# Kernel tuning notes

Measured on AMD Instinct MI355X. Metric: run time of the kernel, lower is better.

The kernel has to match this reference:

```python
import jax, jax.numpy as jnp
import numpy as np
from math import ceil

N, C_IN, HV, WV = 4, 3, 256, 256
C, K, NUM_LAYERS = 16, 3, 10
HK, WK = 45, 45
PROX_SCALE, KSCALE, KBSCALE, EPS = 10.0, 100.0, 0.01, 1e-8


def conv2_same(x, w):
    # torch F.conv2d (cross-correlation) with 'same' padding
    return jax.lax.conv_general_dilated(x, w, (1, 1), 'SAME',
                                        dimension_numbers=('NCHW', 'OIHW', 'NCHW'))


def pad_to(x, size):
    h, w = x.shape[-2], x.shape[-1]
    pads = [(0, 0)] * (x.ndim - 2) + [(0, size[0] - h), (0, size[1] - w)]
    return jnp.pad(x, pads)


def soft_threshold(x, b):
    return jnp.sign(x) * jax.nn.relu(jnp.abs(x) - b)


def circ_shift(x, s):
    return jnp.roll(x, (-s[0], -s[1]), axis=(-2, -1))


def csq(c):
    return (c * jnp.conj(c)).real


def forward(blurred_image, w0, ws, biases, kernel_biases, kernel_proxes, zetas, eta):
    Nb, C_in, Hv, Wv = blurred_image.shape
    Hs, Ws = Hv + HK - 1, Wv + WK - 1
    Hb, Wb = Hs + HK - 1, Ws + WK - 1
    fft_size = (int(ceil(Hb / 64.0) * 64), int(ceil(Wb / 64.0) * 64))
    rfft = lambda x: jnp.fft.rfft2(x, s=fft_size, axes=(-2, -1))
    irfft = lambda X: jnp.fft.irfft2(X, s=fft_size, axes=(-2, -1))

    # first-layer filter: zero-mean per (out,in) filter, then spatial reflect
    w_mean = w0.reshape(C, C_in, -1).mean(axis=-1)
    w0c = w0 - w_mean[:, :, None, None]
    w0_unreflected = jnp.transpose(w0c, (1, 0, 2, 3))   # (C_in, C, K, K)
    w0r = w0c[:, :, ::-1, ::-1]

    # analysis: cascade of convs, each feature stack padded to fft_size
    wy_list = []
    fy = blurred_image
    for layer in range(NUM_LAYERS):
        w = w0r if layer == 0 else ws[layer - 1]
        fy = conv2_same(fy, w)
        fy_p = pad_to(jnp.pad(fy, ((0, 0), (0, 0), (HK - 1, HK - 1), (WK - 1, WK - 1))), fft_size)
        wy_list.append(fy_p)

    delta = jnp.zeros((Nb, HK, WK), dtype=blurred_image.dtype).at[:, HK // 2, WK // 2].set(1.0)
    b0 = biases[0][None, :, None, None]
    z = soft_threshold(circ_shift(wy_list[-1], (HK // 2, WK // 2)), b0)
    Fz = rfft(z)
    k = delta
    Fg = None
    for layer in range(NUM_LAYERS):
        fy_p = wy_list.pop()
        Ffy = rfft(fy_p)                       # (N, C, H, Wf) complex
        Fk = rfft(k)[:, None]                  # (N, 1, H, Wf)
        zeta = PROX_SCALE * zetas[layer][None, :, None, None]
        num = zeta * (jnp.conj(Fk) * Ffy) + Fz
        den = zeta * csq(Fk) + 1.0
        Fg = num / (den + EPS)
        b = biases[layer + 1][None, :, None, None]
        z = soft_threshold(irfft(Fg), b)
        Fz = rfft(z)
        zk = kernel_proxes[layer]
        num_k = zk * jnp.sum(jnp.conj(Fz) * Ffy, axis=1) + Fk[:, 0]
        den_k = zk * jnp.sum(csq(Fz), axis=1) + 1.0
        k = irfft(num_k / (den_k + EPS))
        k_flat = k.reshape(Nb, -1)
        k_max = jax.scipy.special.logsumexp(k_flat * KSCALE, axis=-1) / KSCALE
        bk = KBSCALE * kernel_biases[layer]
        k = jax.nn.relu(k[:, :HK, :WK] - bk * k_max[:, None, None])
        k_sum = jnp.sum(k, axis=(1, 2), keepdims=True)
        k = (k + EPS * delta) / (k_sum + EPS)

    # final closed-form image solve in frequency domain (3-channel Cramer's rule)
    Fy = rfft(jnp.pad(blurred_image, ((0, 0), (0, 0), (HK - 1, HK - 1), (WK - 1, WK - 1))))
    Fk = rfft(k)                                # (N, H, Wf)
    Fw0 = rfft(circ_shift(pad_to(w0_unreflected, fft_size), (K // 2, K // 2)))  # (C_in, C, H, Wf)
    b_final = biases[NUM_LAYERS + 1][None, :, None, None]
    Fg = rfft(soft_threshold(irfft(Fg), b_final))

    eta_s = PROX_SCALE * eta[None, :, None, None]      # (1, C, 1, 1)
    Fwr, Fwg, Fwb = Fw0[0:1], Fw0[1:2], Fw0[2:3]       # (1, C, H, Wf)
    Fyr, Fyg, Fyb = Fy[:, 0], Fy[:, 1], Fy[:, 2]
    Fk_sq = csq(Fk)
    Crr = Fk_sq + jnp.sum(eta_s * csq(Fwr), axis=1)
    Cgg = Fk_sq + jnp.sum(eta_s * csq(Fwg), axis=1)
    Cbb = Fk_sq + jnp.sum(eta_s * csq(Fwb), axis=1)
    Crg = jnp.sum(eta_s * jnp.conj(Fwr) * Fwg, axis=1)
    Crb = jnp.sum(eta_s * jnp.conj(Fwr) * Fwb, axis=1)
    Cgb = jnp.sum(eta_s * jnp.conj(Fwg) * Fwb, axis=1)
    Fk_conj = jnp.conj(Fk)
    Br = Fk_conj * Fyr + jnp.sum(eta_s * jnp.conj(Fwr) * Fg, axis=1)
    Bg = Fk_conj * Fyg + jnp.sum(eta_s * jnp.conj(Fwg) * Fg, axis=1)
    Bb = Fk_conj * Fyb + jnp.sum(eta_s * jnp.conj(Fwb) * Fg, axis=1)
    Crg_sq, Crb_sq, Cgb_sq = csq(Crg), csq(Crb), csq(Cgb)
    Irr = Cgg * Cbb - Cgb_sq
    Igg = Crr * Cbb - Crb_sq
    Ibb = Crr * Cgg - Crg_sq
    Irg = jnp.conj(Cgb) * Crb - Cbb * Crg
    Irb = Crg * Cgb - Cgg * Crb
    Igb = jnp.conj(Crg) * Crb - Crr * Cgb
    den = (Crr * (Cgg * Cbb - Cgb_sq) - Cgg * Crb_sq - Cbb * Crg_sq
           + 2 * (Crg * Cgb * jnp.conj(Crb)).real) + EPS
    Fxr = Irr * Br + Irg * Bg + Irb * Bb
    Fxg = jnp.conj(Irg) * Br + Igg * Bg + Igb * Bb
    Fxb = jnp.conj(Irb) * Br + jnp.conj(Igb) * Bg + Ibb * Bb
    Fx = jnp.stack([Fxr, Fxg, Fxb], axis=1) / den[:, None]

    image = irfft(Fx)[:, :, HK // 2:HK // 2 + Hv, WK // 2:WK // 2 + Wv]
    return image, k


def setup_inputs() -> dict:
    key = jax.random.key(0)
    ks = jax.random.split(key, 4)

    def xavier(k, shape, fan_in, fan_out):
        std = (2.0 / (fan_in + fan_out)) ** 0.5
        return std * jax.random.normal(k, shape, dtype=jnp.float32)

    return {
        'blurred_image': jax.random.normal(ks[0], (N, C_IN, HV, WV), dtype=jnp.float32),
        'w0': xavier(ks[1], (C, C_IN, K, K), C_IN * K * K, C * K * K),
        'ws': xavier(ks[2], (NUM_LAYERS - 1, C, C, 3, 3), C * 9, C * 9),
        'biases': jnp.full((NUM_LAYERS + 2, C), 0.02, dtype=jnp.float32),
        'kernel_biases': jnp.zeros((NUM_LAYERS,), dtype=jnp.float32),
        'kernel_proxes': jnp.ones((NUM_LAYERS,), dtype=jnp.float32),
        'zetas': jnp.ones((NUM_LAYERS, C), dtype=jnp.float32),
        'eta': jnp.ones((C,), dtype=jnp.float32),
    }


def reference(blurred_image, w0, ws, biases, kernel_biases, kernel_proxes, zetas, eta):
    return forward(blurred_image, w0, ws, biases, kernel_biases, kernel_proxes, zetas, eta)
```

## Files before the change

kernel.cpp:

```cpp
#include <hip/hip_runtime.h>
#include <math.h>

#define FH 384
#define KF 193
#define KS 384
#define SPW 147456

typedef __attribute__((ext_vector_type(8))) short short8;
typedef __attribute__((ext_vector_type(4))) float f32x4;
typedef unsigned int u32;
typedef unsigned short u16;

static __device__ __forceinline__ float softt(float v, float b) {
    return copysignf(fmaxf(fabsf(v) - b, 0.f), v);
}
static __device__ __forceinline__ u16 bf16_rn(float v) {
    u32 u = __float_as_uint(v);
    u32 r = (u + 0x7FFFu + ((u >> 16) & 1u)) >> 16;
    return (u16)r;
}
static __device__ __forceinline__ float bf16_to_f(u16 h) {
    return __uint_as_float(((u32)h) << 16);
}
static __device__ __forceinline__ float2 ldc(const uint2* __restrict__ S, size_t i) {
    uint2 u = S[i];
    float2 r;
    r.x = __uint_as_float((u.x & 0xffffu) << 16) + __uint_as_float((u.y & 0xffffu) << 16);
    r.y = __uint_as_float(u.x & 0xffff0000u) + __uint_as_float(u.y & 0xffff0000u);
    return r;
}
static __device__ __forceinline__ uint2 packc(float re, float im) {
    u16 hr = bf16_rn(re), hi = bf16_rn(im);
    u16 lr = bf16_rn(re - bf16_to_f(hr)), li = bf16_rn(im - bf16_to_f(hi));
    uint2 o; o.x = (u32)hr | ((u32)hi << 16); o.y = (u32)lr | ((u32)li << 16);
    return o;
}

__global__ void init_ef_k(float2* Ef) {
    int idx = blockIdx.x * 256 + threadIdx.x;
    if (idx >= FH * FH) return;
    int h = idx / FH, j = idx % FH;
    int m = (h * j) % FH;
    float th = (float)(6.283185307179586 / FH) * (float)m;
    float2 v; v.x = cosf(th); v.y = -sinf(th);
    Ef[idx] = v;
}

__global__ void init_tw(float2* twT) {
    int i = blockIdx.x * 256 + threadIdx.x;
    if (i < 193) {
        float th = (float)(6.283185307179586 / 384.0) * (float)i;
        float2 v; v.x = cosf(th); v.y = sinf(th);
        twT[i] = v;
    }
}

__global__ void init_estack192(u16* __restrict__ H, u16* __restrict__ L, int inv)
{
    int idx = blockIdx.x * 256 + threadIdx.x;
    if (idx >= KS * KS) return;
    int gm = idx / KS, kp = idx % KS;
    int m = gm >> 1, comp = gm & 1;
    int t = kp >> 1, ri = kp & 1;
    int mm = (m * t) % 192;
    float th = (float)(6.283185307179586 / 192.0) * (float)mm;
    float c = cosf(th), s = sinf(th);
    float er, ei;
    if (inv) { er = c * (1.f/384.f); ei = s * (1.f/384.f); }
    else     { er = c;               ei = -s; }
    float v;
    if (comp == 0) v = (ri == 0) ? er : -ei;
    else           v = (ri == 0) ? ei :  er;
    u16 h = bf16_rn(v);
    H[idx] = h;
    L[idx] = bf16_rn(v - bf16_to_f(h));
}

__global__ void init_t192(u16* __restrict__ H, u16* __restrict__ L)
{
    int idx = blockIdx.x * 256 + threadIdx.x;
    if (idx >= 208 * 192) return;
    int n = idx / 192, m = idx % 192;
    float v = 0.f;
    if (n < 194) {
        int j = n >> 1, ri = n & 1;
        int mm = (j * m) % 192;
        float th = (float)(6.283185307179586 / 192.0) * (float)mm;
        v = ri ? -sinf(th) : cosf(th);
    }
    u16 h = bf16_rn(v);
    H[idx] = h;
    L[idx] = bf16_rn(v - bf16_to_f(h));
}

__global__ void init_u192(u16* __restrict__ H, u16* __restrict__ L)
{
    int idx = blockIdx.x * 256 + threadIdx.x;
    if (idx >= 192 * 224) return;
    int m = idx / 224, kk = idx % 224;
    float v = 0.f;
    if (kk < 194) {
        int j = kk >> 1, ri = kk & 1;
        float cj = (j == 0 || j == 96) ? (1.f/384.f) : (2.f/384.f);
        int mm = (j * m) % 192;
        float th = (float)(6.283185307179586 / 192.0) * (float)mm;
        v = ri ? -cj*sinf(th) : cj*cosf(th);
    }
    u16 h = bf16_rn(v);
// ... 249 lines not shown
#pragma unroll
    for (int mi = 0; mi < 2; ++mi)
#pragma unroll
        for (int nj = 0; nj < 4; ++nj) {
            accA[mi][nj] = (f32x4){0.f,0.f,0.f,0.f};
            accB[mi][nj] = (f32x4){0.f,0.f,0.f,0.f};
        }
    const u16* hP = Hs + (size_t)plane*inH*inW;
    const u16* lP = Ls + (size_t)plane*inH*inW;
    int W2  = inW >> 1;
    int ox2 = offX >> 1;
    bool al16 = ((ox2 & 7) == 0);
    int mhi = (offX + inW) >> 1;
    for (int kt = 0; kt < mhi; kt += 32) {
#pragma unroll
        for (int s = 0; s < 4; ++s) {
            int slot = tid + s*256;
            int p    = slot >> 9;
            int inr  = slot & 511;
            int r = inr >> 2, kq2 = inr & 3;
            int yy = y0 + r - offY;
            int m0 = kt + kq2*8;
            int pos = m0 - ox2;
            uint4 hq = {0u,0u,0u,0u}, lq4 = {0u,0u,0u,0u};
            if (yy >= 0 && yy < inH) {
                const u16* hr = hP + (size_t)yy*inW + (size_t)p*W2;
                const u16* lr = lP + (size_t)yy*inW + (size_t)p*W2;
                if (pos >= 0 && pos + 8 <= W2) {
                    if (al16) {
                        hq  = *(const uint4*)(hr + pos);
                        lq4 = *(const uint4*)(lr + pos);
                    } else {
                        hq.x = *(const u32*)(hr+pos);   hq.y = *(const u32*)(hr+pos+2);
                        hq.z = *(const u32*)(hr+pos+4); hq.w = *(const u32*)(hr+pos+6);
                        lq4.x = *(const u32*)(lr+pos);   lq4.y = *(const u32*)(lr+pos+2);
                        lq4.z = *(const u32*)(lr+pos+4); lq4.w = *(const u32*)(lr+pos+6);
                    }
                } else if (pos + 8 > 0 && pos < W2) {
#pragma unroll
                    for (int q = 0; q < 4; ++q) {
                        int pp = pos + 2*q;
                        if (pp >= 0 && pp + 2 <= W2) {
                            ((u32*)&hq)[q]  = *(const u32*)(hr+pp);
                            ((u32*)&lq4)[q] = *(const u32*)(lr+pp);
                        }
                    }
                }
            }
            int base = ((r >> 4)*64 + (r & 15) + 16*kq2)*8;
            *(uint4*)&AhS[p][base] = hq;
            *(uint4*)&AlS[p][base] = lq4;
        }
        __syncthreads();
        short8 A0h[2], A0l[2], A1h[2], A1l[2];
#pragma unroll
        for (int mi = 0; mi < 2; ++mi) {
            int fo = ((wave*2 + mi)*64 + lane)*8;
            A0h[mi] = *(const short8*)&AhS[0][fo];
            A0l[mi] = *(const short8*)&AlS[0][fo];
            A1h[mi] = *(const short8*)&AhS[1][fo];
            A1l[mi] = *(const short8*)&AlS[1][fo];
        }
#pragma unroll
        for (int nj = 0; nj < 4; ++nj) {
            if (nj >= njN) continue;
            size_t toff = (size_t)(col0 + nj*16 + lm)*192 + kt + lq*8;
            short8 Bh = *(const short8*)(TH + toff);
            short8 Bl = *(const short8*)(TL + toff);
#pragma unroll
            for (int mi = 0; mi < 2; ++mi) {
                accA[mi][nj] = __builtin_amdgcn_mfma_f32_16x16x32_bf16(A0h[mi], Bh, accA[mi][nj], 0, 0, 0);
                accA[mi][nj] = __builtin_amdgcn_mfma_f32_16x16x32_bf16(A0h[mi], Bl, accA[mi][nj], 0, 0, 0);
                accA[mi][nj] = __builtin_amdgcn_mfma_f32_16x16x32_bf16(A0l[mi], Bh, accA[mi][nj], 0, 0, 0);
                accB[mi][nj] = __builtin_amdgcn_mfma_f32_16x16x32_bf16(A1h[mi], Bh, accB[mi][nj], 0, 0, 0);
                accB[mi][nj] = __builtin_amdgcn_mfma_f32_16x16x32_bf16(A1h[mi], Bl, accB[mi][nj], 0, 0, 0);
                accB[mi][nj] = __builtin_amdgcn_mfma_f32_16x16x32_bf16(A1l[mi], Bh, accB[mi][nj], 0, 0, 0);
            }
        }
        __syncthreads();
    }
    r2c192_epilogue(accA, accB, col0, njN, y0, wave, lm, lq, twT, outp, B, plane);
}

__global__ void gpm_kernel(uint2* __restrict__ S, const float2* __restrict__ twT, int rows)
{
    int idx = blockIdx.x*256 + threadIdx.x;
    if (idx >= rows * 97) return;
    int j = idx % 97;
    size_t b = (size_t)(idx / 97) * KF;
    if (j == 96) {
        float2 f = ldc(S, b + 96);
        S[b + 96] = packc(2.f*f.x, -2.f*f.y);
    } else {
        float2 f1 = ldc(S, b + j);
        float2 f2 = ldc(S, b + 192 - j);
        float gpx = f1.x + f2.x, gpy = f1.y - f2.y;
        float hx  = f1.x - f2.x, hy  = f1.y + f2.y;
        float2 tw = twT[j];
        float gmx = tw.x*hx - tw.y*hy;
        float gmy = tw.x*hy + tw.y*hx;
        S[b + j]       = packc(gpx, gpy);
        S[b + 192 - j] = packc(gmx, gmy);
    }
}

__global__ __launch_bounds__(256) void c2r192(
    const uint2* __restrict__ Ain,
    const u16* __restrict__ UH, const u16* __restrict__ UL,
    float* __restrict__ outp, const float* __restrict__ thr,
    u16* __restrict__ spH, u16* __restrict__ spL, int B)
{
    __shared__ u16 AhS[2][8*64*8];
    __shared__ u16 AlS[2][8*64*8];
    int col0 = blockIdx.x * 64;
    int y0   = blockIdx.y * 128;
    int plane = blockIdx.z;
    int tid = threadIdx.x;
    int wave = tid >> 6, lane = tid & 63;
    int lm = lane & 15, lq = lane >> 4;
    f32x4 accP[2][4], accQ[2][4];
#pragma unroll
    for (int mi = 0; mi < 2; ++mi)
#pragma unroll
        for (int nj = 0; nj < 4; ++nj) {
            accP[mi][nj] = (f32x4){0.f,0.f,0.f,0.f};
            accQ[mi][nj] = (f32x4){0.f,0.f,0.f,0.f};
        }
    for (int kt = 0; kt < 194; kt += 32) {
#pragma unroll
        for (int s = 0; s < 8; ++s) {
            int slot = tid + s*256;
            int p   = slot >> 10;
            int inr = slot & 1023;
            int r = inr >> 3, kq = inr & 7;
            size_t rowb = ((size_t)(y0 + r)*B + plane)*KF;
            int j0 = (kt + kq*4) >> 1;
            uint2 u0, u1;
            u0.x = u0.y = u1.x = u1.y = 0u;
            if (p == 0) {
                if (j0 < 96) u0 = Ain[rowb + j0];
                else if (j0 == 96) {
                    uint2 t = Ain[rowb + 96];
                    u0.x = t.x & 0xffffu; u0.y = t.y & 0xffffu;
                }
                if (j0 + 1 < 96) u1 = Ain[rowb + j0 + 1];
            } else {
                if (j0 < 96) u0 = Ain[rowb + 192 - j0];
                else if (j0 == 96) {
                    uint2 t = Ain[rowb + 96];
                    u0.x = t.x >> 16; u0.y = t.y >> 16;
                }
                if (j0 + 1 < 96) u1 = Ain[rowb + 191 - j0];
            }
            int base = ((r >> 4)*64 + (r & 15) + 16*(kq >> 1))*8 + (kq & 1)*4;
            uint2 hp, lp;
            hp.x = u0.x; hp.y = u1.x;
            lp.x = u0.y; lp.y = u1.y;
            *(uint2*)&AhS[p][base] = hp;
            *(uint2*)&AlS[p][base] = lp;
        }
        __syncthreads();
        short8 A0h[2], A0l[2], A1h[2], A1l[2];
#pragma unroll
        for (int mi = 0; mi < 2; ++mi) {
            int fo = ((wave*2 + mi)*64 + lane)*8;
            A0h[mi] = *(const short8*)&AhS[0][fo];
            A0l[mi] = *(const short8*)&AlS[0][fo];
            A1h[mi] = *(const short8*)&AhS[1][fo];
            A1l[mi] = *(const short8*)&AlS[1][fo];
        }
#pragma unroll
        for (int nj = 0; nj < 4; ++nj) {
            size_t toff = (size_t)(col0 + nj*16 + lm)*224 + kt + lq*8;
            short8 Bh = *(const short8*)(UH + toff);
            short8 Bl = *(const short8*)(UL + toff);
#pragma unroll
            for (int mi = 0; mi < 2; ++mi) {
                accP[mi][nj] = __builtin_amdgcn_mfma_f32_16x16x32_bf16(A0h[mi], Bh, accP[mi][nj], 0, 0, 0);
                accP[mi][nj] = __builtin_amdgcn_mfma_f32_16x16x32_bf16(A0h[mi], Bl, accP[mi][nj], 0, 0, 0);
                accP[mi][nj] = __builtin_amdgcn_mfma_f32_16x16x32_bf16(A0l[mi], Bh, accP[mi][nj], 0, 0, 0);
                accQ[mi][nj] = __builtin_amdgcn_mfma_f32_16x16x32_bf16(A1h[mi], Bh, accQ[mi][nj], 0, 0, 0);
                accQ[mi][nj] = __builtin_amdgcn_mfma_f32_16x16x32_bf16(A1h[mi], Bl, accQ[mi][nj], 0, 0, 0);
                accQ[mi][nj] = __builtin_amdgcn_mfma_f32_16x16x32_bf16(A1l[mi], Bh, accQ[mi][nj], 0, 0, 0);
            }
        }
        __syncthreads();
    }
    float bthr = thr ? thr[plane & 15] : 0.f;
#pragma unroll
    for (int mi = 0; mi < 2; ++mi) {
#pragma unroll
        for (int nj = 0; nj < 4; ++nj) {
            int m = col0 + nj*16 + lm;
#pragma unroll
            for (int rr = 0; rr < 4; ++rr) {
                int y = y0 + wave*32 + mi*16 + lq*4 + rr;
                float xe = accP[mi][nj][rr];
                float xo = accQ[mi][nj][rr];
                float2 o2; o2.x = xe; o2.y = xo;
                *(float2*)&outp[((size_t)plane*FH + y)*FH + 2*m] = o2;
                if (spH) {
                    float s0 = softt(xe, bthr), s1 = softt(xo, bthr);
                    u16 h0 = bf16_rn(s0), h1 = bf16_rn(s1);
                    u16 l0 = bf16_rn(s0 - bf16_to_f(h0)), l1 = bf16_rn(s1 - bf16_to_f(h1));
                    size_t d = (size_t)plane*SPW + (size_t)y*FH + m;
                    spH[d]       = h0; spL[d]       = l0;
                    spH[d + 192] = h1; spL[d + 192] = l1;
                }
            }
        }
    }
}

__global__ __launch_bounds__(256) void zgemm_col_mfma2(
    const u16* __restrict__ EH, const u16* __restrict__ EL,
    const uint2* __restrict__ Bm, uint2* __restrict__ Cm, int N, float sgn,
    int ktHi, const float2* __restrict__ twT)
{
    __shared__ u16 BhS[2][4*64*8];
    __shared__ u16 BlS[2][4*64*8];
    int col0 = blockIdx.x * 64;
    int row0 = blockIdx.y * 128;
    int tid = threadIdx.x;
    int wave = tid >> 6, lane = tid & 63;
    int lm = lane & 15, lq = lane >> 4;
    f32x4 accE[2][4], accO[2][4];
#pragma unroll
    for (int mi = 0; mi < 2; ++mi)
#pragma unroll
        for (int nj = 0; nj < 4; ++nj) {
            accE[mi][nj] = (f32x4){0.f,0.f,0.f,0.f};
            accO[mi][nj] = (f32x4){0.f,0.f,0.f,0.f};
        }
    int arow0 = row0 + wave*32 + lm;
    for (int kt = 0; kt < ktHi; kt += 32) {
        int tbase = kt >> 1;
#pragma unroll
        for (int s = 0; s < 4; ++s) {
            int slot = tid + s*256;
            int p    = slot >> 9;
            int inr  = slot & 511;
            int pair = inr >> 6;
            int n    = inr & 63;
            int gn   = col0 + n;
            int t0   = tbase + pair*2;
            uint2 u0, u1;
            u0.x = u0.y = u1.x = u1.y = 0u;
            if (gn < N) {
                u0 = Bm[(size_t)(2*t0 + p)*N + gn];
                u1 = Bm[(size_t)(2*t0 + 2 + p)*N + gn];
            }
            int ntile = n >> 4, n0 = n & 15;
            int lrow  = (pair >> 1)*16 + n0;
            int base  = (ntile*64 + lrow)*8 + (pair & 1)*4;
            uint2 hp, lp;
            hp.x = u0.x; hp.y = u1.x;
            lp.x = u0.y; lp.y = u1.y;
            *(uint2*)&BhS[p][base] = hp;
            *(uint2*)&BlS[p][base] = lp;
        }
        __syncthreads();
        short8 Ah[2], Al[2];
#pragma unroll
        for (int mi = 0; mi < 2; ++mi) {
            size_t aoff = (size_t)(arow0 + mi*16)*KS + kt + lq*8;
            Ah[mi] = *(const short8*)(EH + aoff);
            Al[mi] = *(const short8*)(EL + aoff);
        }
#pragma unroll
        for (int nj = 0; nj < 4; ++nj) {
            short8 Bh0 = *(const short8*)&BhS[0][(nj*64 + lane)*8];
            short8 Bl0 = *(const short8*)&BlS[0][(nj*64 + lane)*8];
            short8 Bh1 = *(const short8*)&BhS[1][(nj*64 + lane)*8];
            short8 Bl1 = *(const short8*)&BlS[1][(nj*64 + lane)*8];
#pragma unroll
            for (int mi = 0; mi < 2; ++mi) {
                accE[mi][nj] = __builtin_amdgcn_mfma_f32_16x16x32_bf16(Ah[mi], Bh0, accE[mi][nj], 0, 0, 0);
                accE[mi][nj] = __builtin_amdgcn_mfma_f32_16x16x32_bf16(Ah[mi], Bl0, accE[mi][nj], 0, 0, 0);
                accE[mi][nj] = __builtin_amdgcn_mfma_f32_16x16x32_bf16(Al[mi], Bh0, accE[mi][nj], 0, 0, 0);
                accO[mi][nj] = __builtin_amdgcn_mfma_f32_16x16x32_bf16(Ah[mi], Bh1, accO[mi][nj], 0, 0, 0);
                accO[mi][nj] = __builtin_amdgcn_mfma_f32_16x16x32_bf16(Ah[mi], Bl1, accO[mi][nj], 0, 0, 0);
                accO[mi][nj] = __builtin_amdgcn_mfma_f32_16x16x32_bf16(Al[mi], Bh1, accO[mi][nj], 0, 0, 0);
            }
        }
        __syncthreads();
    }
#pragma unroll
    for (int mi = 0; mi < 2; ++mi) {
#pragma unroll
        for (int nj = 0; nj < 4; ++nj) {
            int coln = col0 + nj*16 + lm;
            if (coln < N) {
                int r0 = row0 + wave*32 + mi*16 + lq*4;
                int h  = r0 >> 1;
#pragma unroll
                for (int pp = 0; pp < 2; ++pp) {
                    float e_re = accE[mi][nj][2*pp],   e_im = accE[mi][nj][2*pp+1];
                    float o_re = accO[mi][nj][2*pp],   o_im = accO[mi][nj][2*pp+1];
                    int hh = h + pp;
                    float2 tw = twT[hh];
                    float twr = tw.x, twi = sgn * tw.y;
                    float tr = twr*o_re - twi*o_im;
                    float ti = twr*o_im + twi*o_re;
                    Cm[(size_t)hh*N + coln]         = packc(e_re + tr, e_im + ti);
                    Cm[(size_t)(hh + 192)*N + coln] = packc(e_re - tr, e_im - ti);
                }
            }
        }
    }
}

__global__ void fg_kernel(const uint2* __restrict__ Ffy, uint2* __restrict__ Fz,
                          const uint2* __restrict__ Fk, const float* __restrict__ zetas,
                          int L, int total)
{
    int idx = blockIdx.x*256 + threadIdx.x;
    if (idx >= total) return;
    int k = idx % KF; int r = idx / KF;
    int c = r & 15; int hi = r >> 4;
    float zeta = 10.f * zetas[L*16 + c];
    float2 fk = ldc(Fk, (size_t)hi*KF + k);
    float2 fy = ldc(Ffy, idx);
    float2 fz = ldc(Fz, idx);
    float nx = zeta*(fk.x*fy.x + fk.y*fy.y) + fz.x;
    float ny = zeta*(fk.x*fy.y - fk.y*fy.x) + fz.y;
    float den = zeta*(fk.x*fk.x + fk.y*fk.y) + 1.f + 1e-8f;
    float inv = 1.f/den;
    Fz[idx] = packc(nx*inv, ny*inv);
}

__global__ void knum_kernel(const uint2* __restrict__ Fz, const uint2* __restrict__ Ffy,
                            const uint2* __restrict__ Fk, const float* __restrict__ kprox,
                            int L, int total, uint2* __restrict__ outk)
{
    int idx = blockIdx.x*256 + threadIdx.x;
    if (idx >= total) return;
    int k = idx % KF; int r = idx / KF;
    float zk = kprox[L];
    float s1x = 0.f, s1y = 0.f, s2 = 0.f;
    for (int c = 0; c < 16; ++c) {
        size_t bi = ((size_t)r*16 + c)*KF + k;
        float2 fz = ldc(Fz, bi), fy = ldc(Ffy, bi);
        s1x += fz.x*fy.x + fz.y*fy.y;
        s1y += fz.x*fy.y - fz.y*fy.x;
        s2  += fz.x*fz.x + fz.y*fz.y;
    }
    float2 fk = ldc(Fk, idx);
    float nx = zk*s1x + fk.x, ny = zk*s1y + fk.y;
    float den = zk*s2 + 1.f + 1e-8f;
    float inv = 1.f/den;
    outk[idx] = packc(nx*inv, ny*inv);
}

__device__ __forceinline__ void lse_comb(float& m, float& s, float m2, float s2)
{
    if (m2 > m) { s = s * expf(m - m2) + s2; m = m2; }
    else        { s = s + s2 * expf(m2 - m); }
}

__global__ __launch_bounds__(256) void lse_part_kernel(const float* __restrict__ kraw0,
                                                       float2* __restrict__ parts)
{
    int img = blockIdx.y;
    const float* kraw = kraw0 + (size_t)img*FH*FH;
    int b = blockIdx.x, t = threadIdx.x;
    float m = -1e30f, s = 0.f;
    for (int i = b*256 + t; i < FH*FH; i += 64*256) {
        float v = 100.f * kraw[i];
        lse_comb(m, s, v, 1.f);
    }
    __shared__ float sm[256], ss[256];
    sm[t] = m; ss[t] = s;
    __syncthreads();
    for (int st = 128; st > 0; st >>= 1) {
        if (t < st) {
            float mm = sm[t], sc = ss[t];
            lse_comb(mm, sc, sm[t+st], ss[t+st]);
            sm[t] = mm; ss[t] = sc;
        }
        __syncthreads();
    }
    if (t == 0) { float2 o; o.x = sm[0]; o.y = ss[0]; parts[img*64 + b] = o; }
}

__global__ void zero_kernel(float* __restrict__ p, int n)
{
    int i = blockIdx.x*256 + threadIdx.x;
    if (i < n) p[i] = 0.f;
}

__global__ void kdelta_kernel(float* __restrict__ kful, int G)
{
    int t = threadIdx.x;
    if (t < G) kful[(size_t)t*FH*FH + 22*FH + 22] = 1.f;
}

__global__ __launch_bounds__(256) void knew_kernel(const float2* __restrict__ parts,
    const float* __restrict__ kraw0, const float* __restrict__ kb, int L,
    float* __restrict__ kful0)
{
    int img = blockIdx.x;
    const float* kraw = kraw0 + (size_t)img*FH*FH;
    float*       kful = kful0 + (size_t)img*FH*FH;
    int t = threadIdx.x;
    __shared__ float sm[64], ss[64];
    if (t < 64) { float2 p = parts[img*64 + t]; sm[t] = p.x; ss[t] = p.y; }
    __syncthreads();
    for (int st = 32; st > 0; st >>= 1) {
        if (t < st) {
            float mm = sm[t], sc = ss[t];
            lse_comb(mm, sc, sm[t+st], ss[t+st]);
            sm[t] = mm; ss[t] = sc;
        }
        __syncthreads();
    }
    float kmax = (sm[0] + logf(ss[0])) * 0.01f;
    float thr = 0.01f * kb[L] * kmax;
    float vs[8]; float loc = 0.f;
#pragma unroll
    for (int ii = 0; ii < 8; ++ii) {
        int i = t + ii*256;
        float v = 0.f;
        if (i < 45*45) {
            int y = i/45, x = i - y*45;
            v = fmaxf(kraw[y*FH + x] - thr, 0.f);
        }
        vs[ii] = v; loc += v;
    }
    __shared__ float sr[256];
    sr[t] = loc; __syncthreads();
    for (int st = 128; st > 0; st >>= 1) { if (t < st) sr[t] += sr[t+st]; __syncthreads(); }
    float den = sr[0] + 1e-8f;
#pragma unroll
    for (int ii = 0; ii < 8; ++ii) {
        int i = t + ii*256;
        if (i < 45*45) {
            int y = i/45, x = i - y*45;
            float v = vs[ii] + ((y == 22 && x == 22) ? 1e-8f : 0.f);
            kful[y*FH + x] = v / den;
        }
    }
}

__global__ void fw0_kernel(const float* __restrict__ w0c, const float2* __restrict__ Ef,
                           float2* __restrict__ Fw0)
{
    int idx = blockIdx.x*256 + threadIdx.x;
    if (idx >= 48*FH*KF) return;
    int k = idx % KF; int r = idx / KF;
    int c = r & 15; int r2 = r >> 4;
    int ci = r2 % 3; int h = r2 / 3;
    float accx = 0.f, accy = 0.f;
#pragma unroll
    for (int ky = 0; ky < 3; ++ky) {
        int a1 = ky - 1; if (a1 < 0) a1 += FH;
        float2 e1 = Ef[h*FH + a1];
#pragma unroll
        for (int kx = 0; kx < 3; ++kx) {
            int a2 = kx - 1; if (a2 < 0) a2 += FH;
            float2 e2 = Ef[k*FH + a2];
            float wv = w0c[((c*3 + ci)*3 + ky)*3 + kx];
            float tr = e1.x*e2.x - e1.y*e2.y;
            float ti = e1.x*e2.y + e1.y*e2.x;
            accx += wv*tr; accy += wv*ti;
        }
    }
    float2 o; o.x = accx; o.y = accy;
    Fw0[idx] = o;
}

__global__ void wiener_kernel(const uint2* __restrict__ Fk, const uint2* __restrict__ Fy,
    const float2* __restrict__ Fw0, const uint2* __restrict__ Fg2,
    const float* __restrict__ eta, int G, int total, uint2* __restrict__ Fx)
{
    int idx = blockIdx.x*256 + threadIdx.x;
    if (idx >= total) return;
    int k = idx % KF; int r = idx / KF;
    int h = r / G;
    float2 fk = ldc(Fk, idx);
    float fksq = fk.x*fk.x + fk.y*fk.y;
    float2 fyr = ldc(Fy, ((size_t)3*r + 0)*KF + k);
    float2 fyg = ldc(Fy, ((size_t)3*r + 1)*KF + k);
    float2 fyb = ldc(Fy, ((size_t)3*r + 2)*KF + k);
    float Crr = fksq, Cgg = fksq, Cbb = fksq;
    float2 Crg, Crb, Cgb;
    Crg.x = Crg.y = Crb.x = Crb.y = Cgb.x = Cgb.y = 0.f;
    float2 Br, Bg, Bb;
    Br.x = fk.x*fyr.x + fk.y*fyr.y; Br.y = fk.x*fyr.y - fk.y*fyr.x;
    Bg.x = fk.x*fyg.x + fk.y*fyg.y; Bg.y = fk.x*fyg.y - fk.y*fyg.x;
    Bb.x = fk.x*fyb.x + fk.y*fyb.y; Bb.y = fk.x*fyb.y - fk.y*fyb.x;
    for (int c = 0; c < 16; ++c) {
// ... 6 lines not shown
        Cgg += es*(wg.x*wg.x + wg.y*wg.y);
        Cbb += es*(wb.x*wb.x + wb.y*wb.y);
        Crg.x += es*(wr.x*wg.x + wr.y*wg.y); Crg.y += es*(wr.x*wg.y - wr.y*wg.x);
        Crb.x += es*(wr.x*wb.x + wr.y*wb.y); Crb.y += es*(wr.x*wb.y - wr.y*wb.x);
        Cgb.x += es*(wg.x*wb.x + wg.y*wb.y); Cgb.y += es*(wg.x*wb.y - wg.y*wb.x);
        Br.x += es*(wr.x*g.x + wr.y*g.y); Br.y += es*(wr.x*g.y - wr.y*g.x);
        Bg.x += es*(wg.x*g.x + wg.y*g.y); Bg.y += es*(wg.x*g.y - wg.y*g.x);
        Bb.x += es*(wb.x*g.x + wb.y*g.y); Bb.y += es*(wb.x*g.y - wb.y*g.x);
    }
    float Crg_sq = Crg.x*Crg.x + Crg.y*Crg.y;
    float Crb_sq = Crb.x*Crb.x + Crb.y*Crb.y;
    float Cgb_sq = Cgb.x*Cgb.x + Cgb.y*Cgb.y;
    float Irr = Cgg*Cbb - Cgb_sq;
    float Igg = Crr*Cbb - Crb_sq;
    float Ibb = Crr*Cgg - Crg_sq;
    float2 Irg, Irb, Igb;
    Irg.x = (Cgb.x*Crb.x + Cgb.y*Crb.y) - Cbb*Crg.x;
    Irg.y = (Cgb.x*Crb.y - Cgb.y*Crb.x) - Cbb*Crg.y;
    Irb.x = (Crg.x*Cgb.x - Crg.y*Cgb.y) - Cgg*Crb.x;
    Irb.y = (Crg.x*Cgb.y + Crg.y*Cgb.x) - Cgg*Crb.y;
    Igb.x = (Crg.x*Crb.x + Crg.y*Crb.y) - Crr*Cgb.x;
    Igb.y = (Crg.x*Crb.y - Crg.y*Crb.x) - Crr*Cgb.y;
    float tx_ = Crg.x*Cgb.x - Crg.y*Cgb.y;
    float ty_ = Crg.x*Cgb.y + Crg.y*Cgb.x;
    float den = Crr*Irr - Cgg*Crb_sq - Cbb*Crg_sq + 2.f*(tx_*Crb.x + ty_*Crb.y) + 1e-8f;
    float inv = 1.f/den;
    float ox, oy;
    ox = (Irr*Br.x + (Irg.x*Bg.x - Irg.y*Bg.y) + (Irb.x*Bb.x - Irb.y*Bb.y))*inv;
    oy = (Irr*Br.y + (Irg.x*Bg.y + Irg.y*Bg.x) + (Irb.x*Bb.y + Irb.y*Bb.x))*inv;
    Fx[((size_t)3*r + 0)*KF + k] = packc(ox, oy);
    ox = ((Irg.x*Br.x + Irg.y*Br.y) + Igg*Bg.x + (Igb.x*Bb.x - Igb.y*Bb.y))*inv;
    oy = ((Irg.x*Br.y - Irg.y*Br.x) + Igg*Bg.y + (Igb.x*Bb.y + Igb.y*Bb.x))*inv;
    Fx[((size_t)3*r + 1)*KF + k] = packc(ox, oy);
    ox = ((Irb.x*Br.x + Irb.y*Br.y) + (Igb.x*Bg.x + Igb.y*Bg.y) + Ibb*Bb.x)*inv;
    oy = ((Irb.x*Br.y - Irb.y*Br.x) + (Igb.x*Bg.y - Igb.y*Bg.x) + Ibb*Bb.y)*inv;
    Fx[((size_t)3*r + 2)*KF + k] = packc(ox, oy);
}

__global__ void crop_kernel(const float* __restrict__ sp, float* __restrict__ outp, int total)
{
    int idx = blockIdx.x*256 + threadIdx.x;
    if (idx >= total) return;
    int x = idx & 255; int r = idx >> 8; int y = r & 255; int plane = r >> 8;
    outp[idx] = sp[((size_t)plane*FH + (y+22))*FH + (x+22)];
}

__global__ void kcopy_kernel(const float* __restrict__ kful, float* __restrict__ outp, int total)
{
    int idx = blockIdx.x*256 + threadIdx.x;
    if (idx >= total) return;
    int rem = idx % 2025; int img = idx / 2025;
    int x = rem % 45; int y = rem / 45;
    outp[idx] = kful[(size_t)img*FH*FH + y*FH + x];
}

extern "C" void kernel_launch(void* const* d_in, const int* in_sizes, int n_in,
                              void* d_out, int out_size, void* d_ws, size_t ws_size,
                              hipStream_t stream)
{
    (void)in_sizes; (void)n_in; (void)out_size;
    const float* blurred = (const float*)d_in[0];
    const float* w0      = (const float*)d_in[1];
    const float* wsw     = (const float*)d_in[2];
    const float* biases  = (const float*)d_in[3];
    const float* kbias   = (const float*)d_in[4];
    const float* kprox   = (const float*)d_in[5];
    const float* zetas   = (const float*)d_in[6];
    const float* eta     = (const float*)d_in[7];
    float* outp = (float*)d_out;

    auto al = [](size_t b) { return (b + 255) & ~(size_t)255; };
    auto need = [&](int G) -> size_t {
        size_t s = 0;
        s += al((size_t)FH*FH*8);
        s += al(193*8);
        s += 4*al((size_t)KS*KS*2);
        s += 2*al((size_t)208*192*2);
        s += 2*al((size_t)192*224*2);
        s += al(432*4);
        s += 2*al((size_t)10*G*16*65536*2);
        s += al((size_t)G*16*FH*FH*4);
        s += 2*al((size_t)G*16*SPW*2);
        s += 3*al((size_t)G*16*FH*KF*8);
        s += 3*al((size_t)G*FH*KF*8);
        s += 2*al((size_t)G*FH*FH*4);
        s += 2*al((size_t)G*3*FH*KF*8);
        s += al((size_t)G*64*8);
        return s;
    };
    int G = 4;
    while (G > 1 && need(G) > ws_size) G >>= 1;

    char* base = (char*)d_ws;
    size_t off = 0;
    auto alloc = [&](size_t bytes) -> void* {
        void* p = (void*)(base + off);
        off += (bytes + 255) & ~(size_t)255;
        return p;
    };
    float2* Ef   = (float2*)alloc((size_t)FH*FH*8);
    float2* twT  = (float2*)alloc(193*8);
    u16* EfH = (u16*)alloc((size_t)KS*KS*2);
    u16* EfL = (u16*)alloc((size_t)KS*KS*2);
    u16* EiH = (u16*)alloc((size_t)KS*KS*2);
    u16* EiL = (u16*)alloc((size_t)KS*KS*2);
    u16* T1H = (u16*)alloc((size_t)208*192*2);
    u16* T1L = (u16*)alloc((size_t)208*192*2);
    u16* U1H = (u16*)alloc((size_t)192*224*2);
    u16* U1L = (u16*)alloc((size_t)192*224*2);
    float*  w0cB = (float*)alloc(432*4);
    u16*    fyH  = (u16*)alloc((size_t)10*G*16*65536*2);
    u16*    fyL  = (u16*)alloc((size_t)10*G*16*65536*2);
    float*  zsp  = (float*)alloc((size_t)G*16*FH*FH*4);
    u16*    zspSH= (u16*)alloc((size_t)G*16*SPW*2);
    u16*    zspSL= (u16*)alloc((size_t)G*16*SPW*2);
    uint2*  mid  = (uint2*)alloc((size_t)G*16*FH*KF*8);
    uint2*  FzFg = (uint2*)alloc((size_t)G*16*FH*KF*8);
    uint2*  Ffy  = (uint2*)alloc((size_t)G*16*FH*KF*8);
    uint2*  Fk   = (uint2*)alloc((size_t)G*FH*KF*8);
    uint2*  kfA  = (uint2*)alloc((size_t)G*FH*KF*8);
    uint2*  kfB  = (uint2*)alloc((size_t)G*FH*KF*8);
    float*  kraw = (float*)alloc((size_t)G*FH*FH*4);
    float*  kful = (float*)alloc((size_t)G*FH*FH*4);
    uint2*  FyB  = (uint2*)alloc((size_t)G*3*FH*KF*8);
    uint2*  FxB  = (uint2*)alloc((size_t)G*3*FH*KF*8);
    float2* lseP = (float2*)alloc((size_t)G*64*8);
    float2* Fw0B = (float2*)fyH;

    init_ef_k<<<(FH*FH+255)/256, 256, 0, stream>>>(Ef);
    init_tw<<<1, 256, 0, stream>>>(twT);
    init_estack192<<<(KS*KS+255)/256, 256, 0, stream>>>(EfH, EfL, 0);
    init_estack192<<<(KS*KS+255)/256, 256, 0, stream>>>(EiH, EiL, 1);
    init_t192<<<(208*192+255)/256, 256, 0, stream>>>(T1H, T1L);
    init_u192<<<(192*224+255)/256, 256, 0, stream>>>(U1H, U1L);
    w0c_kernel<<<1, 64, 0, stream>>>(w0, w0cB);

    auto zgf = [&](const uint2* Bm, uint2* Cm, int Ncols) {
        zgemm_col_mfma2<<<dim3((Ncols+63)/64, 3), 256, 0, stream>>>(
            EfH, EfL, Bm, Cm, Ncols, -1.f, KS, twT);
    };
    auto zgi = [&](const uint2* Bm, uint2* Cm, int Ncols) {
        zgemm_col_mfma2<<<dim3((Ncols+63)/64, 3), 256, 0, stream>>>(
            EiH, EiL, Bm, Cm, Ncols, 1.f, KS, twT);
    };
    auto r2c = [&](const float* inp, int inH, int inW, int oY, int oX,
                   const float* thr, uint2* o, int B) {
        r2c192_f<<<dim3(4, 3, B), 256, 0, stream>>>(
            inp, inH, inW, inW, (size_t)inH*inW, oY, oX, thr, T1H, T1L, twT, o, B);
    };
    auto r2cs = [&](const u16* Hs, const u16* Ls, int inH, int inW, int oY, int oX,
                    uint2* o, int B) {
        r2c192_s<<<dim3(4, 3, B), 256, 0, stream>>>(
            Hs, Ls, inH, inW, oY, oX, T1H, T1L, twT, o, B);
    };
    auto c2r = [&](uint2* Ain, float* o, int B,
                   const float* thr, u16* sH, u16* sL) {
        int rows = FH * B;
        gpm_kernel<<<(rows*97 + 255)/256, 256, 0, stream>>>(Ain, twT, rows);
        c2r192<<<dim3(3, 3, B), 256, 0, stream>>>(
            Ain, U1H, U1L, o, thr, sH, sL, B);
    };
    auto r2ck = [&]() {
        r2c192_f<<<dim3(4, 1, G), 256, 0, stream>>>(
            kful, 45, 45, FH, (size_t)FH*FH, 0, 0, nullptr, T1H, T1L, twT, mid, G);
        zgemm_col_mfma2<<<dim3((G*KF+63)/64, 3), 256, 0, stream>>>(
            EfH, EfL, mid, Fk, G*KF, -1.f, 64, twT);
    };

    const size_t CKL = (size_t)G*16*65536;

    for (int g0 = 0; g0 < 4; g0 += G) {
        const float* img = blurred + (size_t)g0*3*65536;

        conv3x3_kernel<<<dim3(16,16,G), 256, 0, stream>>>(
            img, nullptr, nullptr, w0cB, fyH, fyL, 3, 1, (size_t)3*65536);
        for (int l = 1; l < 10; ++l)
            conv3x3_kernel<<<dim3(16,16,G), 256, 0, stream>>>(
                nullptr, fyH + (size_t)(l-1)*CKL, fyL + (size_t)(l-1)*CKL,
                wsw + (size_t)(l-1)*2304,
                fyH + (size_t)l*CKL, fyL + (size_t)l*CKL, 16, 0, (size_t)16*65536);

        int totZ = G*16*FH*FH;
        zinit_kernel<<<(totZ+255)/256, 256, 0, stream>>>(
            fyH + 9*CKL, fyL + 9*CKL, biases, zspSH, zspSL, totZ);
        r2cs(zspSH, zspSL, FH, FH, 0, 0, mid, G*16);
        zgf(mid, FzFg, G*16*KF);

        zero_kernel<<<(G*FH*FH+255)/256, 256, 0, stream>>>(kful, G*FH*FH);
        kdelta_kernel<<<1, 64, 0, stream>>>(kful, G);

        int totS = G*16*FH*KF;
        int totK = G*FH*KF;
        for (int it = 0; it < 10; ++it) {
            int Lfy = 9 - it;
            r2cs(fyH + (size_t)Lfy*CKL, fyL + (size_t)Lfy*CKL, 256, 256, 44, 44, mid, G*16);
            zgf(mid, Ffy, G*16*KF);
            r2ck();
            fg_kernel<<<(totS+255)/256, 256, 0, stream>>>(Ffy, FzFg, Fk, zetas, it, totS);
            zgi(FzFg, mid, G*16*KF);
            c2r(mid, zsp, G*16, biases + (it+1)*16, zspSH, zspSL);
            r2cs(zspSH, zspSL, FH, FH, 0, 0, mid, G*16);
            zgf(mid, FzFg, G*16*KF);
            knum_kernel<<<(totK+255)/256, 256, 0, stream>>>(FzFg, Ffy, Fk, kprox, it, totK, kfA);
            zgi(kfA, kfB, G*KF);
            c2r(kfB, kraw, G, nullptr, nullptr, nullptr);
            lse_part_kernel<<<dim3(64,G), 256, 0, stream>>>(kraw, lseP);
            knew_kernel<<<G, 256, 0, stream>>>(lseP, kraw, kbias, it, kful);
        }

        r2c(img, 256, 256, 44, 44, nullptr, mid, 3*G);
        zgf(mid, FyB, 3*G*KF);
        r2ck();
        r2c(zsp, FH, FH, 0, 0, biases + 11*16, mid, G*16);
        zgf(mid, FzFg, G*16*KF);
        fw0_kernel<<<(48*FH*KF+255)/256, 256, 0, stream>>>(w0cB, Ef, Fw0B);
        wiener_kernel<<<(totK+255)/256, 256, 0, stream>>>(Fk, FyB, Fw0B, FzFg, eta, G, totK, FxB);
        zgi(FxB, mid, 3*G*KF);
        c2r(mid, zsp, 3*G, nullptr, nullptr, nullptr);
        int totC = G*3*65536;
        crop_kernel<<<(totC+255)/256, 256, 0, stream>>>(zsp, outp + (size_t)g0*3*65536, totC);
        int totKC = G*2025;
        kcopy_kernel<<<(totKC+255)/256, 256, 0, stream>>>(kful, outp + 786432 + g0*2025, totKC);
    }
}
```

Measured before the change: 8.726 ms.

## Fuse fg update into column FFT epilogue and LSE partials into c2r

Folds the per-element Fz/Fg Wiener-style update into the epilogue of the forward column FFT GEMM for Ffy, which removes the separate fg_kernel launch and its reread of Ffy. Folds the log-sum-exp partial reduction into the c2r192 epilogue and drops lse_part_kernel, so knew combines 9 partials per image instead of 64. Moves the kernel-FFT r2ck ahead and gives it its own scratch buffer (kmid) so it no longer overwrites mid. It also precomputes the per-slot load indices outside the k loop. The cost is extra registers and global loads in the GEMM epilogue, plus a shared-memory reduction at the end of c2r.

```diff
diff --git a/kernel.cpp b/kernel.cpp
--- a/kernel.cpp
+++ b/kernel.cpp
@@ -24,6 +24,12 @@
 }
 static __device__ __forceinline__ float2 ldc(const uint2* __restrict__ S, size_t i) {
     uint2 u = S[i];
+    float2 r;
+    r.x = __uint_as_float((u.x & 0xffffu) << 16) + __uint_as_float((u.y & 0xffffu) << 16);
+    r.y = __uint_as_float(u.x & 0xffff0000u) + __uint_as_float(u.y & 0xffff0000u);
+    return r;
+}
+static __device__ __forceinline__ float2 ldcu(uint2 u) {
     float2 r;
     r.x = __uint_as_float((u.x & 0xffffu) << 16) + __uint_as_float((u.y & 0xffffu) << 16);
     r.y = __uint_as_float(u.x & 0xffff0000u) + __uint_as_float(u.y & 0xffff0000u);
@@ -439,6 +445,12 @@
     r2c192_epilogue(accA, accB, col0, njN, y0, wave, lm, lq, twT, outp, B, plane);
 }
 
+__device__ __forceinline__ void lse_comb(float& m, float& s, float m2, float s2)
+{
+    if (m2 > m) { s = s * expf(m - m2) + s2; m = m2; }
+    else        { s = s + s2 * expf(m2 - m); }
+}
+
 __global__ void gpm_kernel(uint2* __restrict__ S, const float2* __restrict__ twT, int rows)
 {
     int idx = blockIdx.x*256 + threadIdx.x;
@@ -465,7 +477,8 @@
     const uint2* __restrict__ Ain,
     const u16* __restrict__ UH, const u16* __restrict__ UL,
     float* __restrict__ outp, const float* __restrict__ thr,
-    u16* __restrict__ spH, u16* __restrict__ spL, int B)
+    u16* __restrict__ spH, u16* __restrict__ spL, int B,
+    float2* __restrict__ parts)
 {
     __shared__ u16 AhS[2][8*64*8];
     __shared__ u16 AlS[2][8*64*8];
@@ -544,6 +557,7 @@
         __syncthreads();
     }
     float bthr = thr ? thr[plane & 15] : 0.f;
+    float lm_ = -1e30f, ls_ = 0.f;
 #pragma unroll
     for (int mi = 0; mi < 2; ++mi) {
 #pragma unroll
@@ -564,7 +578,28 @@
                     spH[d]       = h0; spL[d]       = l0;
                     spH[d + 192] = h1; spL[d + 192] = l1;
                 }
-            }
+                if (parts) {
+                    lse_comb(lm_, ls_, 100.f*xe, 1.f);
+                    lse_comb(lm_, ls_, 100.f*xo, 1.f);
+                }
+            }
+        }
+    }
+    if (parts) {
+        __shared__ float sm[256], ss[256];
+        sm[tid] = lm_; ss[tid] = ls_;
+        __syncthreads();
+        for (int st = 128; st > 0; st >>= 1) {
+            if (tid < st) {
+                float mm = sm[tid], sc = ss[tid];
+                lse_comb(mm, sc, sm[tid+st], ss[tid+st]);
+                sm[tid] = mm; ss[tid] = sc;
+            }
+            __syncthreads();
+        }
+        if (tid == 0) {
+            float2 o; o.x = sm[0]; o.y = ss[0];
+            parts[plane*9 + blockIdx.y*3 + blockIdx.x] = o;
         }
     }
 }
@@ -572,7 +607,9 @@
 __global__ __launch_bounds__(256) void zgemm_col_mfma2(
     const u16* __restrict__ EH, const u16* __restrict__ EL,
     const uint2* __restrict__ Bm, uint2* __restrict__ Cm, int N, float sgn,
-    int ktHi, const float2* __restrict__ twT)
+    int ktHi, const float2* __restrict__ twT,
+    uint2* __restrict__ FzFg, const uint2* __restrict__ FkB,
+    const float* __restrict__ zet16, int GKF)
 {
     __shared__ u16 BhS[2][4*64*8];
     __shared__ u16 BlS[2][4*64*8];
@@ -581,6 +618,18 @@
     int tid = threadIdx.x;
     int wave = tid >> 6, lane = tid & 63;
     int lm = lane & 15, lq = lane >> 4;
+    int p_[4], pair_[4], gn_[4];
+    bool ok_[4];
+#pragma unroll
+    for (int s = 0; s < 4; ++s) {
+        int slot = tid + s*256;
+        p_[s]    = slot >> 9;
+        int inr  = slot & 511;
+        pair_[s] = inr >> 6;
+        int n    = inr & 63;
+        gn_[s]   = col0 + n;
+        ok_[s]   = (gn_[s] < N);
+    }
     f32x4 accE[2][4], accO[2][4];
 #pragma unroll
     for (int mi = 0; mi < 2; ++mi)
@@ -594,19 +643,15 @@
         int tbase = kt >> 1;
 #pragma unroll
         for (int s = 0; s < 4; ++s) {
-            int slot = tid + s*256;
-            int p    = slot >> 9;
-            int inr  = slot & 511;
-            int pair = inr >> 6;
-            int n    = inr & 63;
-            int gn   = col0 + n;
-            int t0   = tbase + pair*2;
+            int p = p_[s], pair = pair_[s], gn = gn_[s];
+            int t0 = tbase + pair*2;
             uint2 u0, u1;
             u0.x = u0.y = u1.x = u1.y = 0u;
-            if (gn < N) {
+            if (ok_[s]) {
                 u0 = Bm[(size_t)(2*t0 + p)*N + gn];
                 u1 = Bm[(size_t)(2*t0 + 2 + p)*N + gn];
             }
+            int n = gn - col0;
             int ntile = n >> 4, n0 = n & 15;
             int lrow  = (pair >> 1)*16 + n0;
             int base  = (ntile*64 + lrow)*8 + (pair & 1)*4;
@@ -650,6 +695,14 @@
             if (coln < N) {
                 int r0 = row0 + wave*32 + mi*16 + lq*4;
                 int h  = r0 >> 1;
+                int planeI = 0, kk = 0, imgI = 0;
+                float zeta = 0.f;
+                if (FzFg) {
+                    planeI = coln / KF;
+                    kk = coln - planeI*KF;
+                    imgI = planeI >> 4;
+                    zeta = 10.f * zet16[planeI & 15];
+                }
 #pragma unroll
                 for (int pp = 0; pp < 2; ++pp) {
                     float e_re = accE[mi][nj][2*pp],   e_im = accE[mi][nj][2*pp+1];
@@ -659,31 +712,28 @@
                     float twr = tw.x, twi = sgn * tw.y;
                     float tr = twr*o_re - twi*o_im;
                     float ti = twr*o_im + twi*o_re;
-                    Cm[(size_t)hh*N + coln]         = packc(e_re + tr, e_im + ti);
-                    Cm[(size_t)(hh + 192)*N + coln] = packc(e_re - tr, e_im - ti);
+                    uint2 pa = packc(e_re + tr, e_im + ti);
+                    uint2 pb = packc(e_re - tr, e_im - ti);
+                    Cm[(size_t)hh*N + coln]         = pa;
+                    Cm[(size_t)(hh + 192)*N + coln] = pb;
+                    if (FzFg) {
+#pragma unroll
+                        for (int e = 0; e < 2; ++e) {
+                            int row = hh + e*192;
+                            float2 fy = ldcu(e ? pb : pa);
+                            float2 fz = ldc(FzFg, (size_t)row*N + coln);
+                            float2 fk = ldc(FkB, (size_t)row*GKF + imgI*KF + kk);
+                            float nx = zeta*(fk.x*fy.x + fk.y*fy.y) + fz.x;
+                            float ny = zeta*(fk.x*fy.y - fk.y*fy.x) + fz.y;
+                            float den = zeta*(fk.x*fk.x + fk.y*fk.y) + 1.f + 1e-8f;
+                            float inv = 1.f/den;
+                            FzFg[(size_t)row*N + coln] = packc(nx*inv, ny*inv);
+                        }
+                    }
                 }
             }
         }
     }
-}
-
-__global__ void fg_kernel(const uint2* __restrict__ Ffy, uint2* __restrict__ Fz,
-                          const uint2* __restrict__ Fk, const float* __restrict__ zetas,
-                          int L, int total)
-{
-    int idx = blockIdx.x*256 + threadIdx.x;
-    if (idx >= total) return;
-    int k = idx % KF; int r = idx / KF;
-    int c = r & 15; int hi = r >> 4;
-    float zeta = 10.f * zetas[L*16 + c];
-    float2 fk = ldc(Fk, (size_t)hi*KF + k);
-    float2 fy = ldc(Ffy, idx);
-    float2 fz = ldc(Fz, idx);
-    float nx = zeta*(fk.x*fy.x + fk.y*fy.y) + fz.x;
-    float ny = zeta*(fk.x*fy.y - fk.y*fy.x) + fz.y;
-    float den = zeta*(fk.x*fk.x + fk.y*fk.y) + 1.f + 1e-8f;
-    float inv = 1.f/den;
-    Fz[idx] = packc(nx*inv, ny*inv);
 }
 
 __global__ void knum_kernel(const uint2* __restrict__ Fz, const uint2* __restrict__ Ffy,
@@ -709,37 +759,6 @@
     outk[idx] = packc(nx*inv, ny*inv);
 }
 
-__device__ __forceinline__ void lse_comb(float& m, float& s, float m2, float s2)
-{
-    if (m2 > m) { s = s * expf(m - m2) + s2; m = m2; }
-    else        { s = s + s2 * expf(m2 - m); }
-}
-
-__global__ __launch_bounds__(256) void lse_part_kernel(const float* __restrict__ kraw0,
-                                                       float2* __restrict__ parts)
-{
-    int img = blockIdx.y;
-    const float* kraw = kraw0 + (size_t)img*FH*FH;
-    int b = blockIdx.x, t = threadIdx.x;
-    float m = -1e30f, s = 0.f;
-    for (int i = b*256 + t; i < FH*FH; i += 64*256) {
-        float v = 100.f * kraw[i];
-        lse_comb(m, s, v, 1.f);
-    }
-    __shared__ float sm[256], ss[256];
-    sm[t] = m; ss[t] = s;
-    __syncthreads();
-    for (int st = 128; st > 0; st >>= 1) {
-        if (t < st) {
-            float mm = sm[t], sc = ss[t];
-            lse_comb(mm, sc, sm[t+st], ss[t+st]);
-            sm[t] = mm; ss[t] = sc;
-        }
-        __syncthreads();
-    }
-    if (t == 0) { float2 o; o.x = sm[0]; o.y = ss[0]; parts[img*64 + b] = o; }
-}
-
 __global__ void zero_kernel(float* __restrict__ p, int n)
 {
     int i = blockIdx.x*256 + threadIdx.x;
@@ -760,10 +779,13 @@
     const float* kraw = kraw0 + (size_t)img*FH*FH;
     float*       kful = kful0 + (size_t)img*FH*FH;
     int t = threadIdx.x;
-    __shared__ float sm[64], ss[64];
-    if (t < 64) { float2 p = parts[img*64 + t]; sm[t] = p.x; ss[t] = p.y; }
+    __shared__ float sm[16], ss[16];
+    if (t < 16) {
+        if (t < 9) { float2 p = parts[img*9 + t]; sm[t] = p.x; ss[t] = p.y; }
+        else       { sm[t] = -1e30f; ss[t] = 0.f; }
+    }
     __syncthreads();
-    for (int st = 32; st > 0; st >>= 1) {
+    for (int st = 8; st > 0; st >>= 1) {
         if (t < st) {
             float mm = sm[t], sc = ss[t];
             lse_comb(mm, sc, sm[t+st], ss[t+st]);
@@ -936,7 +958,7 @@
         s += al((size_t)G*16*FH*FH*4);
         s += 2*al((size_t)G*16*SPW*2);
         s += 3*al((size_t)G*16*FH*KF*8);
-        s += 3*al((size_t)G*FH*KF*8);
+        s += 4*al((size_t)G*FH*KF*8);
         s += 2*al((size_t)G*FH*FH*4);
         s += 2*al((size_t)G*3*FH*KF*8);
         s += al((size_t)G*64*8);
@@ -974,6 +996,7 @@
     uint2*  Fk   = (uint2*)alloc((size_t)G*FH*KF*8);
     uint2*  kfA  = (uint2*)alloc((size_t)G*FH*KF*8);
     uint2*  kfB  = (uint2*)alloc((size_t)G*FH*KF*8);
+    uint2*  kmid = (uint2*)alloc((size_t)G*FH*KF*8);
     float*  kraw = (float*)alloc((size_t)G*FH*FH*4);
     float*  kful = (float*)alloc((size_t)G*FH*FH*4);
     uint2*  FyB  = (uint2*)alloc((size_t)G*3*FH*KF*8);
@@ -991,11 +1014,11 @@
 
     auto zgf = [&](const uint2* Bm, uint2* Cm, int Ncols) {
         zgemm_col_mfma2<<<dim3((Ncols+63)/64, 3), 256, 0, stream>>>(
-            EfH, EfL, Bm, Cm, Ncols, -1.f, KS, twT);
+            EfH, EfL, Bm, Cm, Ncols, -1.f, KS, twT, nullptr, nullptr, nullptr, 0);
     };
     auto zgi = [&](const uint2* Bm, uint2* Cm, int Ncols) {
         zgemm_col_mfma2<<<dim3((Ncols+63)/64, 3), 256, 0, stream>>>(
-            EiH, EiL, Bm, Cm, Ncols, 1.f, KS, twT);
+            EiH, EiL, Bm, Cm, Ncols, 1.f, KS, twT, nullptr, nullptr, nullptr, 0);
     };
     auto r2c = [&](const float* inp, int inH, int inW, int oY, int oX,
                    const float* thr, uint2* o, int B) {
@@ -1008,17 +1031,17 @@
             Hs, Ls, inH, inW, oY, oX, T1H, T1L, twT, o, B);
     };
     auto c2r = [&](uint2* Ain, float* o, int B,
-                   const float* thr, u16* sH, u16* sL) {
+                   const float* thr, u16* sH, u16* sL, float2* parts) {
         int rows = FH * B;
         gpm_kernel<<<(rows*97 + 255)/256, 256, 0, stream>>>(Ain, twT, rows);
         c2r192<<<dim3(3, 3, B), 256, 0, stream>>>(
-            Ain, U1H, U1L, o, thr, sH, sL, B);
+            Ain, U1H, U1L, o, thr, sH, sL, B, parts);
     };
     auto r2ck = [&]() {
         r2c192_f<<<dim3(4, 1, G), 256, 0, stream>>>(
-            kful, 45, 45, FH, (size_t)FH*FH, 0, 0, nullptr, T1H, T1L, twT, mid, G);
+            kful, 45, 45, FH, (size_t)FH*FH, 0, 0, nullptr, T1H, T1L, twT, kmid, G);
         zgemm_col_mfma2<<<dim3((G*KF+63)/64, 3), 256, 0, stream>>>(
-            EfH, EfL, mid, Fk, G*KF, -1.f, 64, twT);
+            EfH, EfL, kmid, Fk, G*KF, -1.f, 64, twT, nullptr, nullptr, nullptr, 0);
     };
 
     const size_t CKL = (size_t)G*16*65536;
@@ -1043,22 +1066,22 @@
         zero_kernel<<<(G*FH*FH+255)/256, 256, 0, stream>>>(kful, G*FH*FH);
         kdelta_kernel<<<1, 64, 0, stream>>>(kful, G);
 
-        int totS = G*16*FH*KF;
         int totK = G*FH*KF;
+        int NS = G*16*KF;
         for (int it = 0; it < 10; ++it) {
             int Lfy = 9 - it;
+            r2ck();
             r2cs(fyH + (size_t)Lfy*CKL, fyL + (size_t)Lfy*CKL, 256, 256, 44, 44, mid, G*16);
-            zgf(mid, Ffy, G*16*KF);
-            r2ck();
-            fg_kernel<<<(totS+255)/256, 256, 0, stream>>>(Ffy, FzFg, Fk, zetas, it, totS);
-            zgi(FzFg, mid, G*16*KF);
-            c2r(mid, zsp, G*16, biases + (it+1)*16, zspSH, zspSL);
+            zgemm_col_mfma2<<<dim3((NS+63)/64, 3), 256, 0, stream>>>(
+                EfH, EfL, mid, Ffy, NS, -1.f, KS, twT,
+                FzFg, Fk, zetas + it*16, G*KF);
+            zgi(FzFg, mid, NS);
+            c2r(mid, zsp, G*16, biases + (it+1)*16, zspSH, zspSL, nullptr);
             r2cs(zspSH, zspSL, FH, FH, 0, 0, mid, G*16);
-            zgf(mid, FzFg, G*16*KF);
+            zgf(mid, FzFg, NS);
             knum_kernel<<<(totK+255)/256, 256, 0, stream>>>(FzFg, Ffy, Fk, kprox, it, totK, kfA);
             zgi(kfA, kfB, G*KF);
-            c2r(kfB, kraw, G, nullptr, nullptr, nullptr);
-            lse_part_kernel<<<dim3(64,G), 256, 0, stream>>>(kraw, lseP);
+            c2r(kfB, kraw, G, nullptr, nullptr, nullptr, lseP);
             knew_kernel<<<G, 256, 0, stream>>>(lseP, kraw, kbias, it, kful);
         }
 
@@ -1070,7 +1093,7 @@
         fw0_kernel<<<(48*FH*KF+255)/256, 256, 0, stream>>>(w0cB, Ef, Fw0B);
         wiener_kernel<<<(totK+255)/256, 256, 0, stream>>>(Fk, FyB, Fw0B, FzFg, eta, G, totK, FxB);
         zgi(FxB, mid, 3*G*KF);
-        c2r(mid, zsp, 3*G, nullptr, nullptr, nullptr);
+        c2r(mid, zsp, 3*G, nullptr, nullptr, nullptr, nullptr);
         int totC = G*3*65536;
         crop_kernel<<<(totC+255)/256, 256, 0, stream>>>(zsp, outp + (size_t)g0*3*65536, totC);
         int totKC = G*2025;
```

Result: slower. 9.073 ms (+4.0%).
